# Optimization experiments

Hardware: AMD Instinct MI355X
Metric: run time of the kernel (lower is better)

The kernel has to match this reference:

```python
import jax, jax.numpy as jnp
import numpy as np

D_MODEL = 1024
N_HEADS = 16
D_HEAD = D_MODEL // N_HEADS
D_FF = 4096
BATCH = 2
SEQ = 2048
EPS = 1e-5


def setup_inputs() -> dict:
    key = jax.random.key(0)
    ks = jax.random.split(key, 8)
    s = 0.02
    x = jax.random.normal(ks[0], (BATCH, SEQ, D_MODEL), dtype=jnp.float32)
    # Per-head projection weights, stacked: [H, d_head, d_model] (torch Linear stores (out,in))
    wq = jax.random.normal(ks[1], (N_HEADS, D_HEAD, D_MODEL), dtype=jnp.float32) * s
    wk = jax.random.normal(ks[2], (N_HEADS, D_HEAD, D_MODEL), dtype=jnp.float32) * s
    wv = jax.random.normal(ks[3], (N_HEADS, D_HEAD, D_MODEL), dtype=jnp.float32) * s
    wo = jax.random.normal(ks[4], (D_MODEL, D_MODEL), dtype=jnp.float32) * s
    w1 = jax.random.normal(ks[5], (D_FF, D_MODEL), dtype=jnp.float32) * s
    w2 = jax.random.normal(ks[6], (D_MODEL, D_FF), dtype=jnp.float32) * s
    ln1_g = jnp.ones((D_MODEL,), jnp.float32)
    ln1_b = jnp.zeros((D_MODEL,), jnp.float32)
    ln2_g = jnp.ones((D_MODEL,), jnp.float32)
    ln2_b = jnp.zeros((D_MODEL,), jnp.float32)
    return {"x": x, "wq": wq, "wk": wk, "wv": wv, "wo": wo,
            "w1": w1, "w2": w2, "ln1_g": ln1_g, "ln1_b": ln1_b,
            "ln2_g": ln2_g, "ln2_b": ln2_b}


def _layer_norm(x, g, b):
    mu = jnp.mean(x, axis=-1, keepdims=True)
    var = jnp.mean(jnp.square(x - mu), axis=-1, keepdims=True)
    return (x - mu) * jax.lax.rsqrt(var + EPS) * g + b


def _mha(h, wq, wk, wv, wo):
    # h: [b,s,d]; wq/wk/wv: [H,dh,d] -> q/k/v: [b,H,s,dh]
    q = jnp.einsum('bsd,hed->bhse', h, wq)
    k = jnp.einsum('bsd,hed->bhse', h, wk)
    v = jnp.einsum('bsd,hed->bhse', h, wv)
    scores = jnp.einsum('bhqe,bhke->bhqk', q, k) / jnp.sqrt(jnp.float32(D_HEAD))
    weights = jax.nn.softmax(scores, axis=-1)
    ctx = jnp.einsum('bhqk,bhke->bhqe', weights, v)  # [b,H,s,dh]
    # concat heads in order (head 0 first) -> [b,s,H*dh]
    concat = jnp.transpose(ctx, (0, 2, 1, 3)).reshape(h.shape[0], h.shape[1], D_MODEL)
    return concat @ wo.T


def reference(x, wq, wk, wv, wo, w1, w2, ln1_g, ln1_b, ln2_g, ln2_b):
    h = _layer_norm(x, ln1_g, ln1_b)
    attn_out = _mha(h, wq, wk, wv, wo)
    h2 = _layer_norm(x + attn_out, ln2_g, ln2_b)
    ff = jax.nn.gelu(h2 @ w1.T, approximate=False) @ w2.T
    return x + ff
```

## Files before the change

### kernel.cpp

```cpp
#include <hip/hip_runtime.h>
#include <hip/hip_bf16.h>
#include <math.h>

typedef __bf16 bf16_t;
typedef __bf16 bf16x8 __attribute__((ext_vector_type(8)));
typedef __bf16 bf16x4 __attribute__((ext_vector_type(4)));
typedef float f32x4 __attribute__((ext_vector_type(4)));
typedef unsigned int u32;
typedef u32 u32x2 __attribute__((ext_vector_type(2)));

#define DM 1024
#define SEQL 2048
#define NTOK 4096
#define QKVN 3072

__device__ __forceinline__ void gload_lds16(const bf16_t* g, bf16_t* l){
  __builtin_amdgcn_global_load_lds((const __attribute__((address_space(1))) void*)g,
                                   (__attribute__((address_space(3))) void*)l, 16, 0, 0);
}
__device__ __forceinline__ u32 ldsoff(const void* p){
  return (u32)(size_t)(__attribute__((address_space(3))) const void*)p;
}
__device__ __forceinline__ u32x2 tr64(u32 byte_off){
  u32x2 d;
  asm volatile("ds_read_b64_tr_b16 %0, %1" : "=v"(d) : "v"(byte_off));
  return d;
}
__device__ __forceinline__ u32 pack2(float a, float b){
  union{ __bf16 h[2]; u32 w; } z;
  z.h[0]=(__bf16)a; z.h[1]=(__bf16)b; return z.w;
}

__global__ __launch_bounds__(256) void prep_kernel(
    const float* __restrict__ wq, const float* __restrict__ wk,
    const float* __restrict__ wv, const float* __restrict__ wo,
    const float* __restrict__ w1, const float* __restrict__ w2,
    const float* __restrict__ x,  const float* __restrict__ g1,
    const float* __restrict__ b1,
    bf16_t* __restrict__ wqkv_b, bf16_t* __restrict__ wo_b,
    bf16_t* __restrict__ w1_b,   bf16_t* __restrict__ w2_b,
    bf16_t* __restrict__ h1)
{
  __shared__ float red[8];
  const int bid = blockIdx.x;
  const int t = threadIdx.x;
  if (bid < 12288){
    const int flat = (bid*256 + t)*4;
    const int seg = flat >> 20;
    const int off1m = flat & 1048575;
    const float* src; bf16_t* dst;
    if (seg < 3){
      src = (seg==0 ? wq : (seg==1 ? wk : wv)) + off1m;
      dst = wqkv_b + flat;
    } else if (seg == 3){
      src = wo + off1m;  dst = wo_b + off1m;
    } else if (seg < 8){
      src = w1 + (flat - 4*1048576);  dst = w1_b + (flat - 4*1048576);
    } else {
      src = w2 + (flat - 8*1048576);  dst = w2_b + (flat - 8*1048576);
    }
    const float4 v = *(const float4*)src;
    bf16x4 o; o[0]=(__bf16)v.x; o[1]=(__bf16)v.y; o[2]=(__bf16)v.z; o[3]=(__bf16)v.w;
    *(bf16x4*)dst = o;
  } else {
    const int row = bid - 12288;
    const float4 v = *(const float4*)(x + (size_t)row*DM + t*4);
    float s  = v.x+v.y+v.z+v.w;
    float sq = v.x*v.x+v.y*v.y+v.z*v.z+v.w*v.w;
    #pragma unroll
    for (int m=1;m<64;m<<=1){ s += __shfl_xor(s,m); sq += __shfl_xor(sq,m); }
    const int w = t>>6;
    if ((t&63)==0){ red[w]=s; red[4+w]=sq; }
    __syncthreads();
    s  = red[0]+red[1]+red[2]+red[3];
    sq = red[4]+red[5]+red[6]+red[7];
    const float mean = s*(1.f/DM);
    const float var  = sq*(1.f/DM) - mean*mean;
    const float rstd = rsqrtf(var + 1e-5f);
    const float4 gg = *(const float4*)(g1 + t*4);
    const float4 bb = *(const float4*)(b1 + t*4);
    bf16x4 o;
    o[0]=(__bf16)((v.x-mean)*rstd*gg.x+bb.x);
    o[1]=(__bf16)((v.y-mean)*rstd*gg.y+bb.y);
    o[2]=(__bf16)((v.z-mean)*rstd*gg.z+bb.z);
    o[3]=(__bf16)((v.w-mean)*rstd*gg.w+bb.w);
    *(bf16x4*)(h1 + (size_t)row*DM + t*4) = o;
  }
}

__global__ __launch_bounds__(256) void lnb_kernel(const bf16_t* __restrict__ in,
    const float* __restrict__ g, const float* __restrict__ bta,
    bf16_t* __restrict__ outp)
{
  const int row = blockIdx.x;
  const int t = threadIdx.x;
  const bf16x4 raw = *(const bf16x4*)(in + (size_t)row*DM + t*4);
  float4 v;
  v.x=(float)raw[0]; v.y=(float)raw[1]; v.z=(float)raw[2]; v.w=(float)raw[3];
  float s  = v.x+v.y+v.z+v.w;
  float sq = v.x*v.x+v.y*v.y+v.z*v.z+v.w*v.w;
  #pragma unroll
  for (int m=1;m<64;m<<=1){ s += __shfl_xor(s,m); sq += __shfl_xor(sq,m); }
  __shared__ float red[8];
  const int w = t>>6;
  if ((t&63)==0){ red[w]=s; red[4+w]=sq; }
  __syncthreads();
  s  = red[0]+red[1]+red[2]+red[3];
  sq = red[4]+red[5]+red[6]+red[7];
  const float mean = s*(1.f/DM);
  const float var  = sq*(1.f/DM) - mean*mean;
  const float rstd = rsqrtf(var + 1e-5f);
  const float4 gg = *(const float4*)(g + t*4);
  const float4 bb = *(const float4*)(bta + t*4);
  bf16x4 o;
  o[0]=(__bf16)((v.x-mean)*rstd*gg.x+bb.x);
  o[1]=(__bf16)((v.y-mean)*rstd*gg.y+bb.y);
  o[2]=(__bf16)((v.z-mean)*rstd*gg.z+bb.z);
  o[3]=(__bf16)((v.w-mean)*rstd*gg.w+bb.w);
  *(bf16x4*)(outp + (size_t)row*DM + t*4) = o;
}

template<int EPI>
__global__ __launch_bounds__(512, 2) void gemm8ph(
    const bf16_t* __restrict__ A, const bf16_t* __restrict__ Bw,
    void* __restrict__ Cout, int N, int K)
{
  __shared__ __align__(16) char ldsb[131072];
  const int tid = threadIdx.x, lane = tid&63, wid = tid>>6;
  const int q16 = lane&15, g = lane>>4;
  const int wm = wid>>2, wn = wid&3;

  const int flat = blockIdx.y*gridDim.x + blockIdx.x;
  const int xcd = flat&7, jj = flat>>3;
  const int NY = gridDim.y;
  const int jdiv = jj/NY, jmod = jj - jdiv*NY;
  const int bm = (xcd*2 + jdiv)*256, bn = jmod*256;

  int mloc, kloc;
  {
    const u32 L = tid*16;
    const u32 logical = L ^ (((L>>9)&1)<<5);
    mloc = (int)(logical>>6);
    kloc = (int)((logical&63)>>1);
  }
  const bf16_t* asrc = A  + (size_t)(bm + mloc)*K + kloc;
  const bf16_t* bsrc = Bw + (size_t)(bn + mloc)*K + kloc;
  const u32 laneOff = ((u32)(q16*64 + g*16)) ^ ((u32)(q16&8)<<2);

  f32x4 acc[8][4] = {};
  bf16x8 bv[4];

  auto stage = [&](int buf, int kh, int isB, int s){
    const bf16_t* src = isB ? bsrc : asrc;
    #pragma unroll
    for (int h2=0; h2<2; h2++)
      gload_lds16(src + (size_t)(h2*128)*K + s*64 + kh*32,
                  (bf16_t*)(ldsb + buf*65536 + isB*32768 + kh*16384 + h2*8192 + tid*16));
  };

  stage(0,0,0,0); stage(0,0,1,0); stage(0,1,0,0); stage(0,1,1,0);
  stage(1,0,0,1); stage(1,0,1,1);
  asm volatile("s_waitcnt vmcnt(4)" ::: "memory");
  __builtin_amdgcn_s_barrier();

  const int NSTEP = K>>6;
  const int NIT = NSTEP>>1;

#define PHASE(BUF,KH,MH,DOST,SBUF,SKH,SISB,SSTEP,CK) { \
    bf16x8 av[4]; \
    const char* Ab_ = ldsb + (BUF)*65536 + (KH)*16384 + wm*8192; \
    _Pragma("unroll") for (int jx=0;jx<4;jx++) \
      av[jx] = *(const bf16x8*)(Ab_ + (((MH)*4+jx)<<10) + laneOff); \
    if ((MH)==0){ \
      const char* Bb_ = ldsb + (BUF)*65536 + 32768 + (KH)*16384 + (wn>>1)*8192; \
      _Pragma("unroll") for (int jx=0;jx<4;jx++) \
        bv[jx] = *(const bf16x8*)(Bb_ + ((((wn&1)*4)+jx)<<10) + laneOff); \
    } \
    if (DOST) stage(SBUF,SKH,SISB,SSTEP); \
    asm volatile("s_barrier" ::: "memory"); \
    asm volatile("s_waitcnt lgkmcnt(0)" ::: "memory"); \
    __builtin_amdgcn_s_setprio(1); \
    _Pragma("unroll") for (int jx=0;jx<4;jx++) \
      _Pragma("unroll") for (int j2=0;j2<4;j2++) \
        acc[(MH)*4+jx][j2] = __builtin_amdgcn_mfma_f32_16x16x32_bf16(av[jx], bv[j2], acc[(MH)*4+jx][j2],0,0,0); \
    __builtin_amdgcn_s_setprio(0); \
    if (CK){ if (nl) { asm volatile("s_waitcnt vmcnt(4)" ::: "memory"); } \
             else    { asm volatile("s_waitcnt vmcnt(0)" ::: "memory"); } } \
    asm volatile("s_barrier" ::: "memory"); }

  for (int it=0; it<NIT; it++){
    const int s0 = 2*it, s1 = s0+1;
    const bool nl = (it+1 < NIT);
    PHASE(0,0,0, 1,  1,1,0, s1,   0)
    PHASE(0,0,1, 1,  1,1,1, s1,   0)
    PHASE(0,1,0, nl, 0,0,0, s0+2, 0)
    PHASE(0,1,1, nl, 0,0,1, s0+2, 1)
    PHASE(1,0,0, nl, 0,1,0, s0+2, 0)
    PHASE(1,0,1, nl, 0,1,1, s0+2, 0)
    PHASE(1,1,0, nl, 1,0,0, s1+2, 0)
    PHASE(1,1,1, nl, 1,0,1, s1+2, 1)
  }
#undef PHASE

  #pragma unroll
  for (int fm=0; fm<8; fm++)
    #pragma unroll
    for (int fn=0; fn<4; fn++)
      #pragma unroll
      for (int i=0; i<4; i++){
        const int r = bm + wm*128 + fm*16 + g*4 + i;
        const int c = bn + wn*64 + fn*16 + q16;
        const size_t idx = (size_t)r*N + c;
        const float vv = acc[fm][fn][i];
        if constexpr (EPI==0){
          ((bf16_t*)Cout)[idx] = (__bf16)vv;
        } else {
          const float ge = 0.5f*vv*(1.0f + erff(vv*0.70710678118654752f));
          ((bf16_t*)Cout)[idx] = (__bf16)ge;
        }
      }
}

template<int EPI>
__global__ __launch_bounds__(512, 2) void gemm128(
    const bf16_t* __restrict__ A, const bf16_t* __restrict__ Bw,
    void* __restrict__ Cout, const float* __restrict__ X,
    int N, int K)
{
  constexpr int BK = 32;
  __shared__ __align__(16) char ldsb[3*16384];
  const int tid = threadIdx.x, lane = tid&63, wid = tid>>6;
  const int q16 = lane&15, g = lane>>4;
  const int wm = wid>>2, wn = wid&3;

  const int flat = blockIdx.y*gridDim.x + blockIdx.x;
  const int xcd = flat&7, j = flat>>3;
  const int bm = ((xcd<<2) + (j>>3))*128, bn = (j&7)*128;

  int mloc, kloc;
  {
    const u32 L = tid*16;
    const u32 logical = L ^ (((L>>9)&1)<<5);
    mloc = (int)(logical>>6);
    kloc = (int)((logical&63)>>1);
  }
  const bf16_t* asrc = A  + (size_t)(bm + mloc)*K + kloc;
  const bf16_t* bsrc = Bw + (size_t)(bn + mloc)*K + kloc;
  const u32 laneOff = ((u32)(q16*64 + g*16)) ^ ((u32)(q16&8)<<2);

  f32x4 acc[4][2] = {};

  auto stageA = [&](int buf, int k0){
    gload_lds16(asrc + k0, (bf16_t*)(ldsb + buf*16384 + tid*16));
  };
  auto stageB = [&](int buf, int k0){
    gload_lds16(bsrc + k0, (bf16_t*)(ldsb + buf*16384 + 8192 + tid*16));
  };

  stageA(0,0); stageB(0,0);
  stageA(1,BK); stageB(1,BK);
  asm volatile("s_waitcnt vmcnt(2)" ::: "memory");
  __builtin_amdgcn_s_barrier();

  const int NT = K/BK;
  int bcur = 0;
  for (int kt=0; kt<NT; kt++){
    const int bstg = (bcur >= 1) ? bcur-1 : bcur+2;
    const char* Ab = ldsb + bcur*16384 + wm*4096;
    const char* Bb = ldsb + bcur*16384 + 8192 + wn*2048;
    const bool sOK = (kt+2 < NT);
    const int k0s = (kt+2)*BK;
    bf16x8 bv[2];
    #pragma unroll
    for (int p=0; p<2; p++){
      bf16x8 av[2];
      #pragma unroll
      for (int jx=0;jx<2;jx++)
        av[jx] = *(const bf16x8*)(Ab + ((p*2+jx)<<10) + laneOff);
      if (p==0){
        #pragma unroll
        for (int jx=0;jx<2;jx++)
          bv[jx] = *(const bf16x8*)(Bb + (jx<<10) + laneOff);
      }
      if (sOK){
        if (p==0) stageA(bstg,k0s);
        else      stageB(bstg,k0s);
      }
      asm volatile("s_barrier" ::: "memory");
      __builtin_amdgcn_s_setprio(1);
      #pragma unroll
      for (int jx=0;jx<2;jx++)
        #pragma unroll
        for (int j2=0;j2<2;j2++)
          acc[p*2+jx][j2] = __builtin_amdgcn_mfma_f32_16x16x32_bf16(av[jx], bv[j2], acc[p*2+jx][j2], 0,0,0);
      __builtin_amdgcn_s_setprio(0);
      if (p==1){
        if (sOK) asm volatile("s_waitcnt vmcnt(2)" ::: "memory");
        else     asm volatile("s_waitcnt vmcnt(0)" ::: "memory");
      }
      asm volatile("s_barrier" ::: "memory");
    }
    bcur = (bcur==2)?0:bcur+1;
  }

  #pragma unroll
  for (int fm=0; fm<4; fm++)
    #pragma unroll
    for (int fn=0; fn<2; fn++)
      #pragma unroll
      for (int i=0; i<4; i++){
        const int r = bm + wm*64 + fm*16 + g*4 + i;
        const int c = bn + wn*32 + fn*16 + q16;
        const size_t idx = (size_t)r*N + c;
        const float vv = X[idx] + acc[fm][fn][i];
        if constexpr (EPI==0) ((bf16_t*)Cout)[idx] = (__bf16)vv;
        else                  ((float*)Cout)[idx] = vv;
      }
}

__global__ __launch_bounds__(512, 4) void attn_kernel(
    const bf16_t* __restrict__ QKV, bf16_t* __restrict__ Ctx)
{
  __shared__ __align__(16) bf16_t Ks[2][64*64];
  __shared__ __align__(16) bf16_t Vs[2][16*4*72];
  const int tid = threadIdx.x, lane = tid&63, w = tid>>6;
  const int g = lane>>4, q16 = lane&15;
  const int bh = blockIdx.y, b = bh>>4, h = bh&15;
  const int qr0 = blockIdx.x*128 + w*16;
  const size_t tok0 = (size_t)b*SEQL;
  const int ch0 = h*64;

  bf16x8 aq[2];
  #pragma unroll
  for (int ks=0; ks<2; ks++){
    bf16x8 t = *(const bf16x8*)(QKV + (tok0+qr0+q16)*QKVN + ch0 + ks*32 + g*8);
    #pragma unroll
    for (int jx=0;jx<8;jx++) t[jx] = (__bf16)((float)t[jx]*0.18033688f);
    aq[ks] = t;
  }

  const int srow = tid>>3, sc8 = (tid&7)*8;
  const bf16_t* kptr_swz = QKV + (tok0+srow)*QKVN + 1024 + ch0 + (sc8 ^ ((srow&7)<<3));
  const bf16_t* vptr = QKV + (tok0+srow)*QKVN + 2048 + ch0 + sc8;
  const int vwoff = ((srow>>2)*4 + (sc8>>4))*72 + (srow&3)*16 + (sc8&15);

  float mrun = -1e30f, lrun = 0.f;
  f32x4 o[4] = {};

  gload_lds16(kptr_swz, &Ks[0][tid*8]);
  bf16x8 vreg = *(const bf16x8*)vptr;
  *(bf16x8*)&Vs[0][vwoff] = vreg;
  vreg = *(const bf16x8*)(vptr + (size_t)64*QKVN);

  const int NT = SEQL/64;
  for (int t=0; t<NT; t++){
    __syncthreads();
    if (t+1 < NT){
      gload_lds16(kptr_swz + (size_t)(t+1)*64*QKVN, &Ks[(t+1)&1][tid*8]);
      *(bf16x8*)&Vs[(t+1)&1][vwoff] = vreg;
      if (t+2 < NT)
        vreg = *(const bf16x8*)(vptr + (size_t)(t+2)*64*QKVN);
    }
    const bf16_t* ksb = Ks[t&1];
    const u32 vs0 = ldsoff(&Vs[t&1][0]);

    f32x4 s[4] = {};
    #pragma unroll
    for (int ks=0; ks<2; ks++){
      #pragma unroll
      for (int fn=0; fn<4; fn++){
        const int r = fn*16 + q16;
        const int ce = ks*32 + g*8;
        bf16x8 bk = *(const bf16x8*)&ksb[r*64 + (ce ^ ((r&7)<<3))];
        s[fn] = __builtin_amdgcn_mfma_f32_16x16x32_bf16(bk, aq[ks], s[fn], 0, 0, 0);
      }
    }

    float m0 = fmaxf(fmaxf(s[0][0],s[0][1]), fmaxf(s[0][2],s[0][3]));
    float m1 = fmaxf(fmaxf(s[1][0],s[1][1]), fmaxf(s[1][2],s[1][3]));
    float m2 = fmaxf(fmaxf(s[2][0],s[2][1]), fmaxf(s[2][2],s[2][3]));
    float m3 = fmaxf(fmaxf(s[3][0],s[3][1]), fmaxf(s[3][2],s[3][3]));
    float mx = fmaxf(fmaxf(m0,m1), fmaxf(m2,m3));
    mx = fmaxf(mx, __shfl_xor(mx,16));
    mx = fmaxf(mx, __shfl_xor(mx,32));

    if (!__all(mx <= mrun + 11.54f)){
      const float mnew = fmaxf(mrun, mx);
      const float alpha = __builtin_amdgcn_exp2f(mrun - mnew);
      #pragma unroll
      for (int i=0;i<4;i++){
        const float ai = __shfl(alpha, g*4+i);
        o[0][i]*=ai; o[1][i]*=ai; o[2][i]*=ai; o[3][i]*=ai;
      }
      lrun *= alpha;
      mrun = mnew;
    }

    float rs = 0.f;
    u32 u[4][2];
    #pragma unroll
    for (int fn=0; fn<4; fn++){
      const float e0=__builtin_amdgcn_exp2f(s[fn][0]-mrun);
      const float e1=__builtin_amdgcn_exp2f(s[fn][1]-mrun);
      const float e2=__builtin_amdgcn_exp2f(s[fn][2]-mrun);
      const float e3=__builtin_amdgcn_exp2f(s[fn][3]-mrun);
      rs += (e0+e1)+(e2+e3);
      u[fn][0] = pack2(e0,e1);
      u[fn][1] = pack2(e2,e3);
    }
    rs += __shfl_xor(rs,16);
    rs += __shfl_xor(rs,32);
    lrun += rs;

    #pragma unroll
    for (int ks=0; ks<2; ks++){
      u32x2 vlo[4], vhi[4];
      #pragma unroll
      for (int ne=0; ne<4; ne++){
        const u32 vb = vs0 + (u32)((((ks*8 + 2*g)*4 + ne)*72 + q16)*2);
        vlo[ne] = tr64(vb);
        vhi[ne] = tr64(vb + 576);
      }
      union { u32 wd[4]; bf16x8 v; } pa;
      #pragma unroll
      for (int jj=0; jj<4; jj++){
        const int src = q16 + ((((g&1)<<1) + (jj>>1))<<4);
        const u32 a0 = (u32)__shfl((int)u[2*ks  ][jj&1], src);
        const u32 a1 = (u32)__shfl((int)u[2*ks+1][jj&1], src);
        pa.wd[jj] = (g&2) ? a1 : a0;
      }
      asm volatile("s_waitcnt lgkmcnt(0)" ::: "memory");
      __builtin_amdgcn_sched_barrier(0);
      union { u32x2 u2[2]; bf16x8 v; } cc;
      #pragma unroll
      for (int ne=0; ne<4; ne++){
        cc.u2[0]=vlo[ne]; cc.u2[1]=vhi[ne];
        o[ne] = __builtin_amdgcn_mfma_f32_16x16x32_bf16(pa.v, cc.v, o[ne], 0, 0, 0);
      }
    }
  }

  const float rl = 1.0f/lrun;
  #pragma unroll
  for (int i=0; i<4; i++){
    const float ri = __shfl(rl, g*4+i);
    #pragma unroll
    for (int ne=0; ne<4; ne++){
      const int r = qr0 + g*4 + i;
      Ctx[(tok0+r)*DM + ch0 + ne*16 + q16] = (__bf16)(o[ne][i]*ri);
    }
  }
}

extern "C" void kernel_launch(void* const* d_in, const int* in_sizes, int n_in,
                              void* d_out, int out_size, void* d_ws, size_t ws_size,
                              hipStream_t stream)
{
  (void)in_sizes; (void)n_in; (void)out_size; (void)ws_size;
  const float* x  = (const float*)d_in[0];
  const float* wq = (const float*)d_in[1];
  const float* wk = (const float*)d_in[2];
  const float* wv = (const float*)d_in[3];
  const float* wo = (const float*)d_in[4];
  const float* w1 = (const float*)d_in[5];
  const float* w2 = (const float*)d_in[6];
  const float* g1 = (const float*)d_in[7];
  const float* b1 = (const float*)d_in[8];
  const float* g2 = (const float*)d_in[9];
  const float* b2 = (const float*)d_in[10];
  float* out = (float*)d_out;
  char* ws = (char*)d_ws;
  const size_t MB = 1024ull*1024ull;

  bf16_t* wqkv_b = (bf16_t*)(ws);
  bf16_t* wo_b   = (bf16_t*)(ws + 6*MB);
  bf16_t* w1_b   = (bf16_t*)(ws + 8*MB);
  bf16_t* w2_b   = (bf16_t*)(ws + 16*MB);
  bf16_t* h1     = (bf16_t*)(ws + 24*MB);
  bf16_t* qkv    = (bf16_t*)(ws + 32*MB);
  bf16_t* ctx    = (bf16_t*)(ws + 56*MB);
  bf16_t* res2b  = (bf16_t*)(ws + 64*MB);
  bf16_t* h2     = h1;
  bf16_t* ffm    = (bf16_t*)(ws + 32*MB);

  prep_kernel<<<16384, 256, 0, stream>>>(wq, wk, wv, wo, w1, w2, x, g1, b1,
                                         wqkv_b, wo_b, w1_b, w2_b, h1);
  gemm8ph<0><<<dim3(16, 12), 512, 0, stream>>>(h1, wqkv_b, (void*)qkv, QKVN, 1024);
  attn_kernel<<<dim3(16, 32), 512, 0, stream>>>(qkv, ctx);
  gemm128<0><<<dim3(32, 8), 512, 0, stream>>>(ctx, wo_b, (void*)res2b, x, 1024, 1024);
  lnb_kernel<<<NTOK, 256, 0, stream>>>(res2b, g2, b2, h2);
  gemm8ph<2><<<dim3(16, 16), 512, 0, stream>>>(h2, w1_b, (void*)ffm, 4096, 1024);
  gemm128<1><<<dim3(32, 8), 512, 0, stream>>>(ffm, w2_b, (void*)out, x, 1024, 4096);
}
```

Measured before the change: 249.4 us.

## Split-K the FFN down-projection with 4-way partials and halve attention block size

The final FFN down-projection GEMM (K=4096) now runs as four independent K=1024 slices through the large-tile gemm8ph kernel. Each slice writes bf16 partials into reused workspace regions, and a new reduction kernel sums the partials with the residual x into fp32 output. The attention kernel moves from 512-thread blocks covering 128 query rows to 256-thread blocks covering 64 rows, with each thread staging two K/V rows, which doubles the grid. The goal is better tile efficiency and occupancy. The cost is extra memory traffic for the partial writes and reads, and precision loss from rounding the partials to bf16.

```diff
diff --git a/kernel.cpp b/kernel.cpp
--- a/kernel.cpp
+++ b/kernel.cpp
@@ -120,10 +120,31 @@
   *(bf16x4*)(outp + (size_t)row*DM + t*4) = o;
 }
 
+__global__ __launch_bounds__(256) void red4_kernel(
+    const bf16_t* __restrict__ p0, const bf16_t* __restrict__ p1,
+    const bf16_t* __restrict__ p2, const bf16_t* __restrict__ p3,
+    const float* __restrict__ x, float* __restrict__ outp)
+{
+  const int i = (blockIdx.x*256 + threadIdx.x)*4;
+  const bf16x4 a0 = *(const bf16x4*)(p0 + i);
+  const bf16x4 a1 = *(const bf16x4*)(p1 + i);
+  const bf16x4 a2 = *(const bf16x4*)(p2 + i);
+  const bf16x4 a3 = *(const bf16x4*)(p3 + i);
+  const float4 xs = *(const float4*)(x + i);
+  float4 o;
+  o.x = xs.x + ((float)a0[0]+(float)a1[0]) + ((float)a2[0]+(float)a3[0]);
+  o.y = xs.y + ((float)a0[1]+(float)a1[1]) + ((float)a2[1]+(float)a3[1]);
+  o.z = xs.z + ((float)a0[2]+(float)a1[2]) + ((float)a2[2]+(float)a3[2]);
+  o.w = xs.w + ((float)a0[3]+(float)a1[3]) + ((float)a2[3]+(float)a3[3]);
+  *(float4*)(outp + i) = o;
+}
+
 template<int EPI>
 __global__ __launch_bounds__(512, 2) void gemm8ph(
     const bf16_t* __restrict__ A, const bf16_t* __restrict__ Bw,
-    void* __restrict__ Cout, int N, int K)
+    void* __restrict__ c0, void* __restrict__ c1,
+    void* __restrict__ c2, void* __restrict__ c3,
+    int N, int K, int lda)
 {
   __shared__ __align__(16) char ldsb[131072];
   const int tid = threadIdx.x, lane = tid&63, wid = tid>>6;
@@ -135,6 +156,9 @@
   const int NY = gridDim.y;
   const int jdiv = jj/NY, jmod = jj - jdiv*NY;
   const int bm = (xcd*2 + jdiv)*256, bn = jmod*256;
+  const int sk = blockIdx.z;
+  const int koff = sk*K;
+  void* Cout = (sk==0) ? c0 : (sk==1) ? c1 : (sk==2) ? c2 : c3;
 
   int mloc, kloc;
   {
@@ -143,8 +167,8 @@
     mloc = (int)(logical>>6);
     kloc = (int)((logical&63)>>1);
   }
-  const bf16_t* asrc = A  + (size_t)(bm + mloc)*K + kloc;
-  const bf16_t* bsrc = Bw + (size_t)(bn + mloc)*K + kloc;
+  const bf16_t* asrc = A  + (size_t)(bm + mloc)*lda + koff + kloc;
+  const bf16_t* bsrc = Bw + (size_t)(bn + mloc)*lda + koff + kloc;
   const u32 laneOff = ((u32)(q16*64 + g*16)) ^ ((u32)(q16&8)<<2);
 
   f32x4 acc[8][4] = {};
@@ -154,7 +178,7 @@
     const bf16_t* src = isB ? bsrc : asrc;
     #pragma unroll
     for (int h2=0; h2<2; h2++)
-      gload_lds16(src + (size_t)(h2*128)*K + s*64 + kh*32,
+      gload_lds16(src + (size_t)(h2*128)*lda + s*64 + kh*32,
                   (bf16_t*)(ldsb + buf*65536 + isB*32768 + kh*16384 + h2*8192 + tid*16));
   };
 
@@ -313,12 +337,11 @@
         const int c = bn + wn*32 + fn*16 + q16;
         const size_t idx = (size_t)r*N + c;
         const float vv = X[idx] + acc[fm][fn][i];
-        if constexpr (EPI==0) ((bf16_t*)Cout)[idx] = (__bf16)vv;
-        else                  ((float*)Cout)[idx] = vv;
-      }
-}
-
-__global__ __launch_bounds__(512, 4) void attn_kernel(
+        ((bf16_t*)Cout)[idx] = (__bf16)vv;
+      }
+}
+
+__global__ __launch_bounds__(256, 4) void attn_kernel(
     const bf16_t* __restrict__ QKV, bf16_t* __restrict__ Ctx)
 {
   __shared__ __align__(16) bf16_t Ks[2][64*64];
@@ -326,7 +349,7 @@
   const int tid = threadIdx.x, lane = tid&63, w = tid>>6;
   const int g = lane>>4, q16 = lane&15;
   const int bh = blockIdx.y, b = bh>>4, h = bh&15;
-  const int qr0 = blockIdx.x*128 + w*16;
+  const int qr0 = blockIdx.x*64 + w*16;
   const size_t tok0 = (size_t)b*SEQL;
   const int ch0 = h*64;
 
@@ -347,19 +370,34 @@
   float mrun = -1e30f, lrun = 0.f;
   f32x4 o[4] = {};
 
-  gload_lds16(kptr_swz, &Ks[0][tid*8]);
-  bf16x8 vreg = *(const bf16x8*)vptr;
-  *(bf16x8*)&Vs[0][vwoff] = vreg;
-  vreg = *(const bf16x8*)(vptr + (size_t)64*QKVN);
+  #pragma unroll
+  for (int it=0; it<2; it++)
+    gload_lds16(kptr_swz + (size_t)(it*32)*QKVN, &Ks[0][(tid + it*256)*8]);
+  bf16x8 vreg[2];
+  #pragma unroll
+  for (int it=0; it<2; it++)
+    vreg[it] = *(const bf16x8*)(vptr + (size_t)(it*32)*QKVN);
+  #pragma unroll
+  for (int it=0; it<2; it++)
+    *(bf16x8*)&Vs[0][vwoff + it*2304] = vreg[it];
+  #pragma unroll
+  for (int it=0; it<2; it++)
+    vreg[it] = *(const bf16x8*)(vptr + (size_t)(64 + it*32)*QKVN);
 
   const int NT = SEQL/64;
   for (int t=0; t<NT; t++){
     __syncthreads();
     if (t+1 < NT){
-      gload_lds16(kptr_swz + (size_t)(t+1)*64*QKVN, &Ks[(t+1)&1][tid*8]);
-      *(bf16x8*)&Vs[(t+1)&1][vwoff] = vreg;
-      if (t+2 < NT)
-        vreg = *(const bf16x8*)(vptr + (size_t)(t+2)*64*QKVN);
+      #pragma unroll
+      for (int it=0; it<2; it++){
+        gload_lds16(kptr_swz + (size_t)((t+1)*64 + it*32)*QKVN, &Ks[(t+1)&1][(tid + it*256)*8]);
+        *(bf16x8*)&Vs[(t+1)&1][vwoff + it*2304] = vreg[it];
+      }
+      if (t+2 < NT){
+        #pragma unroll
+        for (int it=0; it<2; it++)
+          vreg[it] = *(const bf16x8*)(vptr + (size_t)((t+2)*64 + it*32)*QKVN);
+      }
     }
     const bf16_t* ksb = Ks[t&1];
     const u32 vs0 = ldsoff(&Vs[t&1][0]);
@@ -482,13 +520,21 @@
   bf16_t* res2b  = (bf16_t*)(ws + 64*MB);
   bf16_t* h2     = h1;
   bf16_t* ffm    = (bf16_t*)(ws + 32*MB);
+  bf16_t* p0     = (bf16_t*)(ws);
+  bf16_t* p1     = (bf16_t*)(ws + 8*MB);
+  bf16_t* p2     = (bf16_t*)(ws + 24*MB);
+  bf16_t* p3     = (bf16_t*)(ws + 64*MB);
 
   prep_kernel<<<16384, 256, 0, stream>>>(wq, wk, wv, wo, w1, w2, x, g1, b1,
                                          wqkv_b, wo_b, w1_b, w2_b, h1);
-  gemm8ph<0><<<dim3(16, 12), 512, 0, stream>>>(h1, wqkv_b, (void*)qkv, QKVN, 1024);
-  attn_kernel<<<dim3(16, 32), 512, 0, stream>>>(qkv, ctx);
+  gemm8ph<0><<<dim3(16, 12), 512, 0, stream>>>(h1, wqkv_b, (void*)qkv, (void*)qkv,
+                                               (void*)qkv, (void*)qkv, QKVN, 1024, 1024);
+  attn_kernel<<<dim3(32, 32), 256, 0, stream>>>(qkv, ctx);
   gemm128<0><<<dim3(32, 8), 512, 0, stream>>>(ctx, wo_b, (void*)res2b, x, 1024, 1024);
   lnb_kernel<<<NTOK, 256, 0, stream>>>(res2b, g2, b2, h2);
-  gemm8ph<2><<<dim3(16, 16), 512, 0, stream>>>(h2, w1_b, (void*)ffm, 4096, 1024);
-  gemm128<1><<<dim3(32, 8), 512, 0, stream>>>(ffm, w2_b, (void*)out, x, 1024, 4096);
-}
+  gemm8ph<2><<<dim3(16, 16), 512, 0, stream>>>(h2, w1_b, (void*)ffm, (void*)ffm,
+                                               (void*)ffm, (void*)ffm, 4096, 1024, 1024);
+  gemm8ph<0><<<dim3(16, 4, 4), 512, 0, stream>>>(ffm, w2_b, (void*)p0, (void*)p1,
+                                                 (void*)p2, (void*)p3, 1024, 1024, 4096);
+  red4_kernel<<<4096, 256, 0, stream>>>(p0, p1, p2, p3, x, out);
+}
```

Result: no change. 254.4 us (+2.0%).
